# Performance work log

Measured on AMD Instinct MI355X. Metric: run time of the kernel, lower is better.

Reference implementation:

```python
import jax, jax.numpy as jnp
import numpy as np

D_IN = 16
D_OUT = 8
HIDDEN = 64


def setup_inputs() -> dict:
    key = jax.random.key(0)
    ks = jax.random.split(key, 8)
    B = 524288
    x = jax.random.normal(ks[0], (B, D_IN), dtype=jnp.float32)
    # scalar attention weights for the two attention blocks, shape [2, 1]
    wq = jax.random.normal(ks[1], (2, 1), dtype=jnp.float32)
    wk = jax.random.normal(ks[2], (2, 1), dtype=jnp.float32)
    wv = jax.random.normal(ks[3], (2, 1), dtype=jnp.float32)
    # hidden: Linear(16 -> HIDDEN), output: Linear(HIDDEN -> 8)
    lim_h = 1.0 / np.sqrt(D_IN)
    Wh = jax.random.uniform(ks[4], (HIDDEN, D_IN), minval=-lim_h, maxval=lim_h, dtype=jnp.float32)
    bh = jax.random.uniform(ks[5], (HIDDEN,), minval=-lim_h, maxval=lim_h, dtype=jnp.float32)
    lim_o = 1.0 / np.sqrt(HIDDEN)
    Wo = jax.random.uniform(ks[6], (D_OUT, HIDDEN), minval=-lim_o, maxval=lim_o, dtype=jnp.float32)
    bo = jax.random.uniform(ks[7], (D_OUT,), minval=-lim_o, maxval=lim_o, dtype=jnp.float32)
    return {"x": x, "wq": wq, "wk": wk, "wv": wv, "Wh": Wh, "bh": bh, "Wo": Wo, "bo": bo}


def _self_attention(x, q, k, v):
    # x: [B, D]; q, k, v: scalars. Q=K=V are scalar-scaled copies of x.
    Q = q * x  # [B, D]
    K = k * x
    V = v * x
    # Alpha[b, i, j] = K[b, i] * Q[b, j]  (outer product, matches Kt @ Q)
    Alpha = K[:, :, None] * Q[:, None, :]  # [B, D, D]
    A = jax.nn.softmax(Alpha, axis=2)
    # O[b, j] = sum_i V[b, i] * A[b, i, j]  (matches V @ AlphaD)
    return jnp.einsum('bi,bij->bj', V, A)  # [B, D]


def reference(x, wq, wk, wv, Wh, bh, Wo, bo):
    o1 = _self_attention(x[:, 0:16], wq[0, 0], wk[0, 0], wv[0, 0])  # [B, 16]
    x1 = jax.nn.sigmoid(o1 @ Wh.T + bh)                              # [B, HIDDEN]
    x2 = x1 @ Wo.T + bo                                              # [B, 8]
    o2 = _self_attention(x2, wq[1, 0], wk[1, 0], wv[1, 0])          # [B, 8]
    w = jax.nn.softmax(o2, axis=1)                                   # [B, 8]
    # out = x[:, None, 8:16] @ w[:, :, None]  -> [B, 1, 1]
    out = jnp.einsum('bi,bi->b', x[:, 8:16], w)[:, None, None]
    return out
```

## Files before the change

kernel.cpp:

```cpp
#include <hip/hip_runtime.h>


typedef float v2f __attribute__((ext_vector_type(2)));

#define LOG2E 1.44269504088896340736f

__device__ __forceinline__ float rcpf(float a) { return __builtin_amdgcn_rcpf(a); }

#if __has_builtin(__builtin_amdgcn_exp2f)
__device__ __forceinline__ float exp2_fast(float a) { return __builtin_amdgcn_exp2f(a); }
#else
__device__ __forceinline__ float exp2_fast(float a) { return __expf(0.6931471805599453f * a); }
#endif

__global__ __launch_bounds__(256) void fused_attn_mlp(
    const float* __restrict__ x,
    const float* __restrict__ wq,
    const float* __restrict__ wk,
    const float* __restrict__ wv,
    const float* __restrict__ Wh,
    const float* __restrict__ bh,
    const float* __restrict__ Wo,
    const float* __restrict__ bo,
    float* __restrict__ out,
    int B)
{
    __shared__ float sWh[64 * 16];
    __shared__ float sWoT[64 * 8];
    __shared__ float sbh[64];

    const int t = threadIdx.x;
    {
        const float4* src = reinterpret_cast<const float4*>(Wh);
        float4* dst = reinterpret_cast<float4*>(sWh);
        dst[t] = src[t];
    }
    #pragma unroll
    for (int r = t; r < 512; r += 256) {
        const int h = r >> 3, o = r & 7;
        sWoT[h * 8 + o] = Wo[o * 64 + h];
    }
    if (t < 64) sbh[t] = bh[t];
    __syncthreads();

    const int b = blockIdx.x * blockDim.x + t;
    if (b >= B) return;

    float xs[16];
    {
        const float4* xr = reinterpret_cast<const float4*>(x) + (size_t)b * 4;
        float4 a0 = xr[0], a1 = xr[1], a2 = xr[2], a3 = xr[3];
        xs[0]=a0.x; xs[1]=a0.y; xs[2]=a0.z; xs[3]=a0.w;
        xs[4]=a1.x; xs[5]=a1.y; xs[6]=a1.z; xs[7]=a1.w;
        xs[8]=a2.x; xs[9]=a2.y; xs[10]=a2.z; xs[11]=a2.w;
        xs[12]=a3.x; xs[13]=a3.y; xs[14]=a3.z; xs[15]=a3.w;
    }
    v2f xv2[8];
    #pragma unroll
    for (int p = 0; p < 8; ++p) { v2f v; v[0] = xs[2*p]; v[1] = xs[2*p+1]; xv2[p] = v; }

    const float kq1 = wk[0] * wq[0] * LOG2E;
    const float v1  = wv[0];

    float xmx = xs[0], xmn = xs[0];
    #pragma unroll
    for (int i = 1; i < 16; ++i) { xmx = fmaxf(xmx, xs[i]); xmn = fminf(xmn, xs[i]); }

    v2f o1v[8];
    #pragma unroll
    for (int p = 0; p < 8; ++p) o1v[p] = (v2f)(0.f);

    #pragma unroll
    for (int i = 0; i < 16; ++i) {
        const float c = kq1 * xs[i];
        const float m = fmaxf(c * xmx, c * xmn);
        v2f cc; cc[0] = c; cc[1] = c;
        v2f mm; mm[0] = m; mm[1] = m;
        v2f e2[8], sv = (v2f)(0.f);
        #pragma unroll
        for (int p = 0; p < 8; ++p) {
            v2f a = cc * xv2[p] - mm;
            v2f e; e[0] = exp2_fast(a[0]); e[1] = exp2_fast(a[1]);
            e2[p] = e;
            sv += e;
        }
        const float s = sv[0] + sv[1];
        const float w = v1 * xs[i] * rcpf(s);
        v2f ww; ww[0] = w; ww[1] = w;
        #pragma unroll
        for (int p = 0; p < 8; ++p) o1v[p] += ww * e2[p];
    }

    v2f x2v[4];
    #pragma unroll
    for (int p = 0; p < 4; ++p) { v2f v; v[0] = bo[2*p]; v[1] = bo[2*p+1]; x2v[p] = v; }

    #pragma unroll 8
    for (int h = 0; h < 64; ++h) {
        const v2f* wh = reinterpret_cast<const v2f*>(sWh + h * 16);
        v2f acc = wh[0] * o1v[0];
        #pragma unroll
        for (int p = 1; p < 8; ++p) acc += wh[p] * o1v[p];
        const float a = acc[0] + acc[1] + sbh[h];
        const float sg = rcpf(1.f + exp2_fast(-a * LOG2E));
        const v2f* wo = reinterpret_cast<const v2f*>(sWoT + h * 8);
        v2f sgv; sgv[0] = sg; sgv[1] = sg;
        #pragma unroll
        for (int p = 0; p < 4; ++p) x2v[p] += wo[p] * sgv;
    }

    const float kq2 = wk[1] * wq[1] * LOG2E;
    const float v2s = wv[1] * LOG2E;

    float ys[8];
    #pragma unroll
    for (int i = 0; i < 8; ++i) ys[i] = x2v[i >> 1][i & 1];
    float ymx = ys[0], ymn = ys[0];
    #pragma unroll
    for (int i = 1; i < 8; ++i) { ymx = fmaxf(ymx, ys[i]); ymn = fminf(ymn, ys[i]); }

    v2f o2v[4];
    #pragma unroll
    for (int p = 0; p < 4; ++p) o2v[p] = (v2f)(0.f);

    #pragma unroll
    for (int i = 0; i < 8; ++i) {
        const float c = kq2 * ys[i];
        const float m = fmaxf(c * ymx, c * ymn);
        v2f cc; cc[0] = c; cc[1] = c;
        v2f mm; mm[0] = m; mm[1] = m;
        v2f e2[4], sv = (v2f)(0.f);
        #pragma unroll
        for (int p = 0; p < 4; ++p) {
            v2f a = cc * x2v[p] - mm;
            v2f e; e[0] = exp2_fast(a[0]); e[1] = exp2_fast(a[1]);
            e2[p] = e;
            sv += e;
        }
        const float s = sv[0] + sv[1];
        const float w = v2s * ys[i] * rcpf(s);
        v2f ww; ww[0] = w; ww[1] = w;
        #pragma unroll
        for (int p = 0; p < 4; ++p) o2v[p] += ww * e2[p];
    }

    float o2s[8];
    #pragma unroll
    for (int i = 0; i < 8; ++i) o2s[i] = o2v[i >> 1][i & 1];
    float m2 = o2s[0];
    #pragma unroll
    for (int i = 1; i < 8; ++i) m2 = fmaxf(m2, o2s[i]);
    float s2 = 0.f, dot = 0.f;
    #pragma unroll
    for (int i = 0; i < 8; ++i) {
        const float e = exp2_fast(o2s[i] - m2);
        s2 += e;
        dot += xs[8 + i] * e;
    }
    out[b] = dot * rcpf(s2);
}

extern "C" void kernel_launch(void* const* d_in, const int* in_sizes, int n_in,
                              void* d_out, int out_size, void* d_ws, size_t ws_size,
                              hipStream_t stream) {
    const float* x  = (const float*)d_in[0];
    const float* wq = (const float*)d_in[1];
    const float* wk = (const float*)d_in[2];
    const float* wv = (const float*)d_in[3];
    const float* Wh = (const float*)d_in[4];
    const float* bh = (const float*)d_in[5];
    const float* Wo = (const float*)d_in[6];
    const float* bo = (const float*)d_in[7];
    float* out = (float*)d_out;

    const int B = in_sizes[0] / 16;
    const int block = 256;
    const int grid = (B + block - 1) / block;
    fused_attn_mlp<<<grid, block, 0, stream>>>(x, wq, wk, wv, Wh, bh, Wo, bo, out, B);
}
```

Baseline: 132.3 us.

## Drop LDS weight staging, batch sigmoid reciprocals, and tree-reduce softmax sums

Removes the shared-memory staging of Wh, Wo and bh and the block barrier, so the hidden layer reads weights straight from global memory as uniform, cache-resident loads. The hidden loop now handles four units at a time and shares one reciprocal across the four sigmoid denominators using a product trick, with the exponent clamped to keep the product finite. Softmax sums become tree reductions and the final softmax is vectorized. Launch bounds now ask for 8 blocks per CU. The risks are higher register pressure under the tighter bound and more global or scalar load traffic for the weights, plus slight numerical change from the clamp and shared reciprocal.

```diff
diff --git a/kernel.cpp b/kernel.cpp
--- a/kernel.cpp
+++ b/kernel.cpp
@@ -13,7 +13,7 @@
 __device__ __forceinline__ float exp2_fast(float a) { return __expf(0.6931471805599453f * a); }
 #endif
 
-__global__ __launch_bounds__(256) void fused_attn_mlp(
+__global__ __launch_bounds__(256, 8) void fused_attn_mlp(
     const float* __restrict__ x,
     const float* __restrict__ wq,
     const float* __restrict__ wk,
@@ -25,28 +25,11 @@
     float* __restrict__ out,
     int B)
 {
-    __shared__ float sWh[64 * 16];
-    __shared__ float sWoT[64 * 8];
-    __shared__ float sbh[64];
-
-    const int t = threadIdx.x;
-    {
-        const float4* src = reinterpret_cast<const float4*>(Wh);
-        float4* dst = reinterpret_cast<float4*>(sWh);
-        dst[t] = src[t];
-    }
-    #pragma unroll
-    for (int r = t; r < 512; r += 256) {
-        const int h = r >> 3, o = r & 7;
-        sWoT[h * 8 + o] = Wo[o * 64 + h];
-    }
-    if (t < 64) sbh[t] = bh[t];
-    __syncthreads();
-
-    const int b = blockIdx.x * blockDim.x + t;
+    const int b = blockIdx.x * blockDim.x + threadIdx.x;
     if (b >= B) return;
 
     float xs[16];
+    v2f xv2[8];
     {
         const float4* xr = reinterpret_cast<const float4*>(x) + (size_t)b * 4;
         float4 a0 = xr[0], a1 = xr[1], a2 = xr[2], a3 = xr[3];
@@ -54,10 +37,9 @@
         xs[4]=a1.x; xs[5]=a1.y; xs[6]=a1.z; xs[7]=a1.w;
         xs[8]=a2.x; xs[9]=a2.y; xs[10]=a2.z; xs[11]=a2.w;
         xs[12]=a3.x; xs[13]=a3.y; xs[14]=a3.z; xs[15]=a3.w;
+        #pragma unroll
+        for (int p = 0; p < 8; ++p) { v2f v; v[0]=xs[2*p]; v[1]=xs[2*p+1]; xv2[p]=v; }
     }
-    v2f xv2[8];
-    #pragma unroll
-    for (int p = 0; p < 8; ++p) { v2f v; v[0] = xs[2*p]; v[1] = xs[2*p+1]; xv2[p] = v; }
 
     const float kq1 = wk[0] * wq[0] * LOG2E;
     const float v1  = wv[0];
@@ -74,39 +56,74 @@
     for (int i = 0; i < 16; ++i) {
         const float c = kq1 * xs[i];
         const float m = fmaxf(c * xmx, c * xmn);
-        v2f cc; cc[0] = c; cc[1] = c;
-        v2f mm; mm[0] = m; mm[1] = m;
-        v2f e2[8], sv = (v2f)(0.f);
+        v2f cc; cc[0]=c; cc[1]=c;
+        v2f mm; mm[0]=m; mm[1]=m;
+        v2f e2[8];
         #pragma unroll
         for (int p = 0; p < 8; ++p) {
             v2f a = cc * xv2[p] - mm;
             v2f e; e[0] = exp2_fast(a[0]); e[1] = exp2_fast(a[1]);
             e2[p] = e;
-            sv += e;
         }
-        const float s = sv[0] + sv[1];
-        const float w = v1 * xs[i] * rcpf(s);
-        v2f ww; ww[0] = w; ww[1] = w;
+        v2f s01 = e2[0] + e2[1];
+        v2f s23 = e2[2] + e2[3];
+        v2f s45 = e2[4] + e2[5];
+        v2f s67 = e2[6] + e2[7];
+        v2f sv  = (s01 + s23) + (s45 + s67);
+        const float w = v1 * xs[i] * rcpf(sv[0] + sv[1]);
+        v2f ww; ww[0]=w; ww[1]=w;
         #pragma unroll
         for (int p = 0; p < 8; ++p) o1v[p] += ww * e2[p];
     }
 
     v2f x2v[4];
     #pragma unroll
-    for (int p = 0; p < 4; ++p) { v2f v; v[0] = bo[2*p]; v[1] = bo[2*p+1]; x2v[p] = v; }
+    for (int p = 0; p < 4; ++p) { v2f v; v[0]=bo[2*p]; v[1]=bo[2*p+1]; x2v[p]=v; }
 
-    #pragma unroll 8
-    for (int h = 0; h < 64; ++h) {
-        const v2f* wh = reinterpret_cast<const v2f*>(sWh + h * 16);
-        v2f acc = wh[0] * o1v[0];
+    const v2f* Wh2 = reinterpret_cast<const v2f*>(Wh);
+
+    #pragma unroll 2
+    for (int g = 0; g < 16; ++g) {
+        float apre[4];
         #pragma unroll
-        for (int p = 1; p < 8; ++p) acc += wh[p] * o1v[p];
-        const float a = acc[0] + acc[1] + sbh[h];
-        const float sg = rcpf(1.f + exp2_fast(-a * LOG2E));
-        const v2f* wo = reinterpret_cast<const v2f*>(sWoT + h * 8);
-        v2f sgv; sgv[0] = sg; sgv[1] = sg;
+        for (int hh = 0; hh < 4; ++hh) {
+            const int h = g * 4 + hh;
+            v2f acc = Wh2[h * 8 + 0] * o1v[0];
+            #pragma unroll
+            for (int p = 1; p < 8; ++p) acc += Wh2[h * 8 + p] * o1v[p];
+            apre[hh] = acc[0] + acc[1] + bh[h];
+        }
+        float d[4];
         #pragma unroll
-        for (int p = 0; p < 4; ++p) x2v[p] += wo[p] * sgv;
+        for (int hh = 0; hh < 4; ++hh) {
+            const float la = fminf(-apre[hh] * LOG2E, 30.f);
+            d[hh] = 1.f + exp2_fast(la);
+        }
+        const float p01  = d[0] * d[1];
+        const float p012 = p01 * d[2];
+        const float rq   = rcpf(p012 * d[3]);
+        const float i3 = rq * p012;
+        const float tq = rq * d[3];
+        const float i2 = tq * p01;
+        const float t2 = tq * d[2];
+        float sg[4];
+        sg[0] = t2 * d[1];
+        sg[1] = t2 * d[0];
+        sg[2] = i2;
+        sg[3] = i3;
+
+        #pragma unroll
+        for (int hh = 0; hh < 4; ++hh) {
+            const int h = g * 4 + hh;
+            v2f sgv; sgv[0] = sg[hh]; sgv[1] = sg[hh];
+            #pragma unroll
+            for (int p = 0; p < 4; ++p) {
+                v2f wo2;
+                wo2[0] = Wo[(2 * p) * 64 + h];
+                wo2[1] = Wo[(2 * p + 1) * 64 + h];
+                x2v[p] += wo2 * sgv;
+            }
+        }
     }
 
     const float kq2 = wk[1] * wq[1] * LOG2E;
@@ -127,19 +144,18 @@
     for (int i = 0; i < 8; ++i) {
         const float c = kq2 * ys[i];
         const float m = fmaxf(c * ymx, c * ymn);
-        v2f cc; cc[0] = c; cc[1] = c;
-        v2f mm; mm[0] = m; mm[1] = m;
-        v2f e2[4], sv = (v2f)(0.f);
+        v2f cc; cc[0]=c; cc[1]=c;
+        v2f mm; mm[0]=m; mm[1]=m;
+        v2f e2[4];
         #pragma unroll
         for (int p = 0; p < 4; ++p) {
             v2f a = cc * x2v[p] - mm;
             v2f e; e[0] = exp2_fast(a[0]); e[1] = exp2_fast(a[1]);
             e2[p] = e;
-            sv += e;
         }
-        const float s = sv[0] + sv[1];
-        const float w = v2s * ys[i] * rcpf(s);
-        v2f ww; ww[0] = w; ww[1] = w;
+        v2f sv = (e2[0] + e2[1]) + (e2[2] + e2[3]);
+        const float w = v2s * ys[i] * rcpf(sv[0] + sv[1]);
+        v2f ww; ww[0]=w; ww[1]=w;
         #pragma unroll
         for (int p = 0; p < 4; ++p) o2v[p] += ww * e2[p];
     }
@@ -150,14 +166,17 @@
     float m2 = o2s[0];
     #pragma unroll
     for (int i = 1; i < 8; ++i) m2 = fmaxf(m2, o2s[i]);
-    float s2 = 0.f, dot = 0.f;
+    v2f mm2; mm2[0]=m2; mm2[1]=m2;
+    v2f se = (v2f)(0.f), de = (v2f)(0.f);
     #pragma unroll
-    for (int i = 0; i < 8; ++i) {
-        const float e = exp2_fast(o2s[i] - m2);
-        s2 += e;
-        dot += xs[8 + i] * e;
+    for (int p = 0; p < 4; ++p) {
+        v2f a = o2v[p] - mm2;
+        v2f e; e[0] = exp2_fast(a[0]); e[1] = exp2_fast(a[1]);
+        se += e;
+        v2f xp; xp[0]=xs[8+2*p]; xp[1]=xs[9+2*p];
+        de += xp * e;
     }
-    out[b] = dot * rcpf(s2);
+    out[b] = (de[0] + de[1]) * rcpf(se[0] + se[1]);
 }
 
 extern "C" void kernel_launch(void* const* d_in, const int* in_sizes, int n_in,
```

New measurement: 135.1 us. +2.1%, slower.
